# Optimization experiments

Hardware: AMD Instinct MI355X
Metric: run time of the kernel (lower is better)

Reference implementation:

```python
import jax, jax.numpy as jnp
import numpy as np

B, S, D_MODEL = 2, 2048, 1024
NUM_HEADS = 16
D_HEAD = D_MODEL // NUM_HEADS
THETA = 10000.0


def setup_inputs() -> dict:
    key = jax.random.key(0)
    ks = jax.random.split(key, 5)
    std = float(np.sqrt(2.0 / (D_MODEL + D_MODEL)))
    return {
        "x": jax.random.normal(ks[0], (B, S, D_MODEL), dtype=jnp.float32),
        "wq": jax.random.normal(ks[1], (D_MODEL, D_MODEL), dtype=jnp.float32) * std,
        "wk": jax.random.normal(ks[2], (D_MODEL, D_MODEL), dtype=jnp.float32) * std,
        "wv": jax.random.normal(ks[3], (D_MODEL, D_MODEL), dtype=jnp.float32) * std,
        "wo": jax.random.normal(ks[4], (D_MODEL, D_MODEL), dtype=jnp.float32) * std,
    }


def _apply_rope(x):
    # x: [b, h, s, d]; interleaved even/odd RoPE rotation
    d = x.shape[-1]
    s = x.shape[-2]
    inv_freq = 1.0 / (THETA ** (jnp.arange(0, d, 2, dtype=x.dtype) / d))  # [d/2]
    pos = jnp.arange(s, dtype=x.dtype)
    freqs = pos[:, None] * inv_freq[None, :]  # [s, d/2]
    cos, sin = jnp.cos(freqs), jnp.sin(freqs)
    x_even = x[..., 0::2]
    x_odd = x[..., 1::2]
    rot_even = x_even * cos - x_odd * sin
    rot_odd = x_even * sin + x_odd * cos
    # interleave back: stack pairs on a new trailing axis then flatten
    return jnp.stack([rot_even, rot_odd], axis=-1).reshape(x.shape)


def reference(x, wq, wk, wv, wo):
    b, s, _ = x.shape
    # Linear applies weight [d_out, d_in] as x @ W^T
    q = jnp.einsum('bsd,ed->bse', x, wq)
    k = jnp.einsum('bsd,ed->bse', x, wk)
    v = jnp.einsum('bsd,ed->bse', x, wv)
    # [b, s, h*dh] -> [b, h, s, dh]
    q = q.reshape(b, s, NUM_HEADS, D_HEAD).transpose(0, 2, 1, 3)
    k = k.reshape(b, s, NUM_HEADS, D_HEAD).transpose(0, 2, 1, 3)
    v = v.reshape(b, s, NUM_HEADS, D_HEAD).transpose(0, 2, 1, 3)
    q = _apply_rope(q)
    k = _apply_rope(k)
    scores = jnp.einsum('bhqd,bhkd->bhqk', q, k) / jnp.sqrt(jnp.asarray(D_HEAD, x.dtype))
    causal = jnp.tril(jnp.ones((s, s), dtype=bool))  # allowed positions
    scores = jnp.where(causal, scores, -jnp.inf)
    attn = jax.nn.softmax(scores, axis=-1)
    out = jnp.einsum('bhqk,bhkd->bhqd', attn, v)
    out = out.transpose(0, 2, 1, 3).reshape(b, s, NUM_HEADS * D_HEAD)
    return jnp.einsum('bsd,ed->bse', out, wo)
```

## Files before the change

kernel.cpp:

```cpp
#include <hip/hip_runtime.h>
#include <stdint.h>

typedef unsigned short u16;
typedef __attribute__((ext_vector_type(8))) short bf16x8;
typedef __attribute__((ext_vector_type(4))) short bf16x4;
typedef __attribute__((ext_vector_type(4))) float f32x4;
typedef __attribute__((ext_vector_type(4))) unsigned short u16x4;
typedef __attribute__((ext_vector_type(2))) unsigned u32x2;

#define S_ 2048
#define E_ 1024
#define QSCALE 0.18033688011112042f

__device__ __forceinline__ u16 f2bf(float f) {
  union { float f; unsigned u; } v; v.f = f;
  unsigned u = v.u;
  unsigned r = (u + 0x7FFFu + ((u >> 16) & 1u)) >> 16;
  return (u16)r;
}
__device__ __forceinline__ float bf2f(u16 h) {
  union { unsigned u; float f; } v; v.u = ((unsigned)h) << 16;
  return v.f;
}
__device__ __forceinline__ unsigned cvtpk(float a, float b) {
  unsigned r;
  asm("v_cvt_pk_bf16_f32 %0, %1, %2" : "=v"(r) : "v"(a), "v"(b));
  return r;
}
__device__ __forceinline__ bf16x4 pk4(float a, float b, float c, float d) {
  union { u32x2 u; bf16x4 v; } U;
  U.u[0] = cvtpk(a, b);
  U.u[1] = cvtpk(c, d);
  return U.v;
}

typedef __attribute__((address_space(3))) void lds_void;
__device__ __forceinline__ unsigned lds_off(void* p) {
  return (unsigned)(unsigned long long)(lds_void*)p;
}
__device__ __forceinline__ void glds16(const u16* g, u16* l) {
  __builtin_amdgcn_global_load_lds(
      (const __attribute__((address_space(1))) void*)g,
      (__attribute__((address_space(3))) void*)l, 16, 0, 0);
}

__global__ void k_cast5(const float* __restrict__ x,
                        const float* __restrict__ wq, const float* __restrict__ wk,
                        const float* __restrict__ wv, const float* __restrict__ wo,
                        u16* __restrict__ xb, u16* __restrict__ wqb, u16* __restrict__ wkb,
                        u16* __restrict__ wvb, u16* __restrict__ wob) {
  int i = blockIdx.x * blockDim.x + threadIdx.x;
  const float* src; u16* dst; int off;
  if (i < 1048576) { src = x; dst = xb; off = i; }
  else {
    int j = i - 1048576;
    int w = j >> 18; off = j & 262143;
    src = (w == 0) ? wq : (w == 1) ? wk : (w == 2) ? wv : wo;
    dst = (w == 0) ? wqb : (w == 1) ? wkb : (w == 2) ? wvb : wob;
  }
  float4 v = *((const float4*)src + off);
  u16x4 o;
  o.x = f2bf(v.x); o.y = f2bf(v.y); o.z = f2bf(v.z); o.w = f2bf(v.w);
  *((u16x4*)dst + off) = o;
}

__global__ __launch_bounds__(256) void k_gemm(
    const u16* __restrict__ A,
    const u16* __restrict__ W0, const u16* __restrict__ W1, const u16* __restrict__ W2,
    void* O0, void* O1, void* O2, int outF32)
{
  __shared__ __align__(16) u16 As[2][128 * 32];
  __shared__ __align__(16) u16 Ws[2][128 * 32];
  int tid = threadIdx.x;
  int wid = tid >> 6, lane = tid & 63;
  int lg = lane >> 4, lr = lane & 15;
  int wsel = blockIdx.y >> 3, nb = blockIdx.y & 7;
  const u16* W = (wsel == 0) ? W0 : ((wsel == 1) ? W1 : W2);
  void* O = (wsel == 0) ? O0 : ((wsel == 1) ? O1 : O2);
  int m0 = blockIdx.x * 128;
  int n0 = nb * 128;
  int wr = wid >> 1, wc = wid & 1;

  f32x4 acc[4][4];
#pragma unroll
  for (int m = 0; m < 4; m++)
#pragma unroll
    for (int n = 0; n < 4; n++) acc[m][n] = (f32x4){0.f, 0.f, 0.f, 0.f};

  int srow = tid >> 2;
  int schunk = (tid & 3) ^ ((tid >> 3) & 3);
  const u16* ag = A + (size_t)(m0 + srow) * 1024 + schunk * 8;
  const u16* wg = W + (size_t)(n0 + srow) * 1024 + schunk * 8;

  int buf = 0;
  glds16(ag, &As[0][tid * 8]);
  glds16(ag + 65536, &As[0][tid * 8 + 2048]);
  glds16(wg, &Ws[0][tid * 8]);
  glds16(wg + 65536, &Ws[0][tid * 8 + 2048]);
  __syncthreads();

  for (int kt = 0; kt < 1024; kt += 32) {
    if (kt + 32 < 1024) {
      glds16(ag + kt + 32, &As[buf ^ 1][tid * 8]);
      glds16(ag + kt + 32 + 65536, &As[buf ^ 1][tid * 8 + 2048]);
      glds16(wg + kt + 32, &Ws[buf ^ 1][tid * 8]);
      glds16(wg + kt + 32 + 65536, &Ws[buf ^ 1][tid * 8 + 2048]);
    }
    bf16x8 af[4], wf[4];
#pragma unroll
    for (int m = 0; m < 4; m++) {
      int row = wr * 64 + m * 16 + lr;
      af[m] = *(const bf16x8*)&As[buf][row * 32 + ((lg ^ ((row >> 1) & 3)) * 8)];
    }
#pragma unroll
    for (int n = 0; n < 4; n++) {
      int row = wc * 64 + n * 16 + lr;
      wf[n] = *(const bf16x8*)&Ws[buf][row * 32 + ((lg ^ ((row >> 1) & 3)) * 8)];
    }
    __builtin_amdgcn_s_setprio(1);
#pragma unroll
    for (int m = 0; m < 4; m++)
#pragma unroll
      for (int n = 0; n < 4; n++)
        acc[m][n] = __builtin_amdgcn_mfma_f32_16x16x32_bf16(af[m], wf[n], acc[m][n], 0, 0, 0);
    __builtin_amdgcn_s_setprio(0);
    __syncthreads();
    buf ^= 1;
  }

#pragma unroll
  for (int m = 0; m < 4; m++) {
    int gr = m0 + wr * 64 + m * 16 + lg * 4;
#pragma unroll
    for (int n = 0; n < 4; n++) {
      int gc = n0 + wc * 64 + n * 16 + lr;
#pragma unroll
      for (int r = 0; r < 4; r++) {
        if (outF32) ((float*)O)[(size_t)(gr + r) * 1024 + gc] = acc[m][n][r];
        else ((u16*)O)[(size_t)(gr + r) * 1024 + gc] = f2bf(acc[m][n][r]);
      }
    }
  }
}

__global__ void k_rope(u16* __restrict__ Q, u16* __restrict__ K) {
  int idx = blockIdx.x * blockDim.x + threadIdx.x;
  int p = idx & 511;
  int srow = idx >> 9;
  int s = srow & (S_ - 1);
  int i = p & 31;
  float ang = (float)s * exp2f(-0.415241012f * (float)i);
  float sn, c;
  __sincosf(ang, &sn, &c);
  unsigned* qp = (unsigned*)Q + idx;
  unsigned qv = *qp;
  float e = bf2f((u16)(qv & 0xffff)), o = bf2f((u16)(qv >> 16));
  float re = (e * c - o * sn) * QSCALE, ro = (e * sn + o * c) * QSCALE;
  *qp = cvtpk(re, ro);
  unsigned* kp = (unsigned*)K + idx;
  unsigned kv = *kp;
  e = bf2f((u16)(kv & 0xffff)); o = bf2f((u16)(kv >> 16));
  re = e * c - o * sn; ro = e * sn + o * c;
  *kp = cvtpk(re, ro);
}

__global__ __launch_bounds__(256) void k_attn(
    const u16* __restrict__ Q, const u16* __restrict__ K,
    const u16* __restrict__ V, u16* __restrict__ AO)
{
  __shared__ __align__(16) u16 Ks[64 * 64];
  __shared__ __align__(16) u16 Vs[64 * 64];
  int tid = threadIdx.x;
  int wid = tid >> 6, lane = tid & 63;
  int lg = lane >> 4, lr = lane & 15;
  int bh = blockIdx.x;
  int by = blockIdx.y;
  int b0 = by & 7, jj = by >> 3;
  int qb = (jj == 0) ? (b0 * 2)
         : (jj == 1) ? (31 - b0 * 2)
         : (jj == 2) ? (b0 * 2 + 1)
                     : (30 - b0 * 2);
  int q0 = qb * 64 + wid * 16;
  size_t base = (size_t)(bh >> 4) * (2048u * 1024u) + (size_t)(bh & 15) * 64;

  const u16* qrow = Q + base + (size_t)(q0 + lr) * 1024 + lg * 8;
  bf16x8 qf0 = *(const bf16x8*)(qrow);
  bf16x8 qf1 = *(const bf16x8*)(qrow + 32);

  int srow = tid >> 3;
  int sch = tid & 7;
  const u16* kg = K + base + (size_t)srow * 1024 + sch * 8;
  const u16* vg = V + base + (size_t)srow * 1024 + sch * 8;
  int kwb0 = ((srow)*128 + sch * 16) ^ ((srow & 7) << 4);
  int kwb1 = ((srow + 32) * 128 + sch * 16) ^ ((srow & 7) << 4);
  int vwi0 = (srow >> 4) * 1024 + (sch >> 1) * 256 + (srow & 15) * 16 + (sch & 1) * 8;
  int vwi1 = ((srow + 32) >> 4) * 1024 + (sch >> 1) * 256 + (srow & 15) * 16 + (sch & 1) * 8;

  bf16x8 kr0 = *(const bf16x8*)(kg);
  bf16x8 kr1 = *(const bf16x8*)(kg + 32 * 1024);
  bf16x8 vr0 = *(const bf16x8*)(vg);
  bf16x8 vr1 = *(const bf16x8*)(vg + 32 * 1024);
  const u16* kgp = kg + 64 * 1024;
  const u16* vgp = vg + 64 * 1024;

  float m = -1e30f, lsum = 0.f;
  f32x4 o[4];
#pragma unroll
  for (int cc = 0; cc < 4; cc++) o[cc] = (f32x4){0.f, 0.f, 0.f, 0.f};

  int qg = q0 + lr;
  int ntile = qb + 1;
  unsigned vrd = lds_off(Vs) + (unsigned)(lane * 8);

  for (int t = 0; t < ntile; ++t) {
    __syncthreads();
    *(bf16x8*)((char*)Ks + kwb0) = kr0;
    *(bf16x8*)((char*)Ks + kwb1) = kr1;
    *(bf16x8*)(&Vs[vwi0]) = vr0;
    *(bf16x8*)(&Vs[vwi1]) = vr1;
    __syncthreads();
    if (t + 1 < ntile) {
      kr0 = *(const bf16x8*)(kgp);
      kr1 = *(const bf16x8*)(kgp + 32 * 1024);
      vr0 = *(const bf16x8*)(vgp);
      vr1 = *(const bf16x8*)(vgp + 32 * 1024);
      kgp += 64 * 1024;
      vgp += 64 * 1024;
    }
    f32x4 sv[4];
    int kv0 = t * 64;
    __builtin_amdgcn_s_setprio(1);
#pragma unroll
    for (int sub = 0; sub < 4; ++sub) {
      int row = sub * 16 + lr;
      int swz = (row & 7) << 4;
      bf16x8 kf0 = *(const bf16x8*)((const char*)Ks + ((row * 128 + lg * 16) ^ swz));
      bf16x8 kf1 = *(const bf16x8*)((const char*)Ks + ((row * 128 + 64 + lg * 16) ^ swz));
      f32x4 z = (f32x4){0.f, 0.f, 0.f, 0.f};
      z = __builtin_amdgcn_mfma_f32_16x16x32_bf16(kf0, qf0, z, 0, 0, 0);
      sv[sub] = __builtin_amdgcn_mfma_f32_16x16x32_bf16(kf1, qf1, z, 0, 0, 0);
    }
    __builtin_amdgcn_s_setprio(0);
    if (t == ntile - 1) {
#pragma unroll
      for (int sub = 0; sub < 4; ++sub)
#pragma unroll
        for (int j = 0; j < 4; ++j) {
          int kvg = kv0 + sub * 16 + lg * 4 + j;
          sv[sub][j] = (kvg <= qg) ? sv[sub][j] : -1e30f;
        }
    }
    float tm = fmaxf(fmaxf(fmaxf(sv[0][0], sv[0][1]), fmaxf(sv[0][2], sv[0][3])),
                     fmaxf(fmaxf(sv[1][0], sv[1][1]), fmaxf(sv[1][2], sv[1][3])));
    tm = fmaxf(tm, fmaxf(fmaxf(fmaxf(sv[2][0], sv[2][1]), fmaxf(sv[2][2], sv[2][3])),
                         fmaxf(fmaxf(sv[3][0], sv[3][1]), fmaxf(sv[3][2], sv[3][3]))));
    tm = fmaxf(tm, __shfl_xor(tm, 16));
    tm = fmaxf(tm, __shfl_xor(tm, 32));
    if (!__all(tm <= m + 8.f)) {
      float mn = fmaxf(m, tm);
      float corr = __builtin_amdgcn_exp2f(m - mn);
      m = mn;
      lsum *= corr;
#pragma unroll
      for (int cc = 0; cc < 4; ++cc) {
        o[cc][0] *= corr; o[cc][1] *= corr; o[cc][2] *= corr; o[cc][3] *= corr;
      }
    }
    bf16x4 pb[4];
#pragma unroll
    for (int sub = 0; sub < 4; ++sub) {
      float p0 = __builtin_amdgcn_exp2f(sv[sub][0] - m);
      float p1 = __builtin_amdgcn_exp2f(sv[sub][1] - m);
      float p2 = __builtin_amdgcn_exp2f(sv[sub][2] - m);
      float p3 = __builtin_amdgcn_exp2f(sv[sub][3] - m);
      lsum += (p0 + p1) + (p2 + p3);
      pb[sub] = pk4(p0, p1, p2, p3);
    }
#pragma unroll
    for (int sub = 0; sub < 4; ++sub) {
      unsigned wa = vrd + (unsigned)(sub * 2048);
      bf16x4 va0, va1, va2, va3;
      asm volatile("ds_read_b64_tr_b16 %0, %1" : "=v"(va0) : "v"(wa));
      asm volatile("ds_read_b64_tr_b16 %0, %1 offset:512" : "=v"(va1) : "v"(wa));
      asm volatile("ds_read_b64_tr_b16 %0, %1 offset:1024" : "=v"(va2) : "v"(wa));
      asm volatile("ds_read_b64_tr_b16 %0, %1 offset:1536" : "=v"(va3) : "v"(wa));
      asm volatile("s_waitcnt lgkmcnt(0)" ::: "memory");
      __builtin_amdgcn_sched_barrier(0);
      __builtin_amdgcn_s_setprio(1);
      o[0] = __builtin_amdgcn_mfma_f32_16x16x16bf16_1k(va0, pb[sub], o[0], 0, 0, 0);
      o[1] = __builtin_amdgcn_mfma_f32_16x16x16bf16_1k(va1, pb[sub], o[1], 0, 0, 0);
      o[2] = __builtin_amdgcn_mfma_f32_16x16x16bf16_1k(va2, pb[sub], o[2], 0, 0, 0);
      o[3] = __builtin_amdgcn_mfma_f32_16x16x16bf16_1k(va3, pb[sub], o[3], 0, 0, 0);
      __builtin_amdgcn_s_setprio(0);
    }
  }

  float lt = lsum + __shfl_xor(lsum, 16);
  lt += __shfl_xor(lt, 32);
  float inv = 1.0f / lt;
  u16* orow = AO + base + (size_t)(q0 + lr) * 1024;
#pragma unroll
  for (int cc = 0; cc < 4; cc++) {
    u32x2 pk;
    pk[0] = cvtpk(o[cc][0] * inv, o[cc][1] * inv);
    pk[1] = cvtpk(o[cc][2] * inv, o[cc][3] * inv);
    *(u32x2*)&orow[cc * 16 + lg * 4] = pk;
  }
}

extern "C" void kernel_launch(void* const* d_in, const int* in_sizes, int n_in,
                              void* d_out, int out_size, void* d_ws, size_t ws_size,
                              hipStream_t stream) {
  const float* x = (const float*)d_in[0];
  const float* wq = (const float*)d_in[1];
  const float* wk = (const float*)d_in[2];
  const float* wv = (const float*)d_in[3];
  const float* wo = (const float*)d_in[4];

  char* ws = (char*)d_ws;
  u16* xb  = (u16*)(ws);
  u16* wqb = (u16*)(ws + 8388608);
  u16* wkb = (u16*)(ws + 10485760);
  u16* wvb = (u16*)(ws + 12582912);
  u16* wob = (u16*)(ws + 14680064);
  u16* Qb  = (u16*)(ws + 16777216);
  u16* Kb  = (u16*)(ws + 25165824);
  u16* Vb  = (u16*)(ws + 33554432);
  u16* AO  = (u16*)(ws + 41943040);

  k_cast5<<<8192, 256, 0, stream>>>(x, wq, wk, wv, wo, xb, wqb, wkb, wvb, wob);
  k_gemm<<<dim3(32, 24), 256, 0, stream>>>(xb, wqb, wkb, wvb, Qb, Kb, Vb, 0);
  k_rope<<<8192, 256, 0, stream>>>(Qb, Kb);
  k_attn<<<dim3(32, 32), 256, 0, stream>>>(Qb, Kb, Vb, AO);
  k_gemm<<<dim3(32, 8), 256, 0, stream>>>(AO, wob, wob, wob, d_out, d_out, d_out, 1);
}
```

Measured before the change: 119.1 us.

## Split causal attention KV range into two halves and merge partial softmax results

Each query block's causal KV tiles are now split into two halves handled by separate workgroups, doubling the attention grid. Each half writes an unnormalized bf16 output plus its running max and sum. A new merge kernel rescales and combines the two partials into the final attention output. The goal is more parallelism and a shorter tail from the longest causal rows. The cost is an extra launch, extra global traffic for the partials, and bf16 rounding of unnormalized accumulators. Freed workspace regions (the casted x and wq buffers) are reused to hold the partials.

```diff
diff --git a/kernel.cpp b/kernel.cpp
--- a/kernel.cpp
+++ b/kernel.cpp
@@ -7,6 +7,7 @@
 typedef __attribute__((ext_vector_type(4))) float f32x4;
 typedef __attribute__((ext_vector_type(4))) unsigned short u16x4;
 typedef __attribute__((ext_vector_type(2))) unsigned u32x2;
+typedef __attribute__((ext_vector_type(4))) unsigned u32x4;
 
 #define S_ 2048
 #define E_ 1024
@@ -166,7 +167,8 @@
 
 __global__ __launch_bounds__(256) void k_attn(
     const u16* __restrict__ Q, const u16* __restrict__ K,
-    const u16* __restrict__ V, u16* __restrict__ AO)
+    const u16* __restrict__ V, u16* __restrict__ AO,
+    u16* __restrict__ P0o, float* __restrict__ P0ml, float* __restrict__ P1ml)
 {
   __shared__ __align__(16) u16 Ks[64 * 64];
   __shared__ __align__(16) u16 Vs[64 * 64];
@@ -175,13 +177,31 @@
   int lg = lane >> 4, lr = lane & 15;
   int bh = blockIdx.x;
   int by = blockIdx.y;
-  int b0 = by & 7, jj = by >> 3;
-  int qb = (jj == 0) ? (b0 * 2)
-         : (jj == 1) ? (31 - b0 * 2)
-         : (jj == 2) ? (b0 * 2 + 1)
-                     : (30 - b0 * 2);
+  int qb = 31 - (by >> 1);
+  int part = by & 1;
+  int ntile = qb + 1;
+  int h = ntile >> 1;
+  int t0 = part ? h : 0;
+  int t1 = part ? ntile : h;
   int q0 = qb * 64 + wid * 16;
   size_t base = (size_t)(bh >> 4) * (2048u * 1024u) + (size_t)(bh & 15) * 64;
+  int mlbase = ((bh >> 4) * 2048) * 16 + (bh & 15);
+
+  u16* Oraw = part ? AO : P0o;
+  float* Pml = part ? P1ml : P0ml;
+
+  if (t0 == t1) {
+    int row = tid >> 2;
+    int col = (tid & 3) * 16;
+    u16* dst = P0o + base + (size_t)row * 1024 + col;
+#pragma unroll
+    for (int j = 0; j < 16; ++j) dst[j] = 0;
+    if (tid < 64) {
+      P0ml[(mlbase + tid * 16) * 2 + 0] = -1e30f;
+      P0ml[(mlbase + tid * 16) * 2 + 1] = 0.f;
+    }
+    return;
+  }
 
   const u16* qrow = Q + base + (size_t)(q0 + lr) * 1024 + lg * 8;
   bf16x8 qf0 = *(const bf16x8*)(qrow);
@@ -189,8 +209,8 @@
 
   int srow = tid >> 3;
   int sch = tid & 7;
-  const u16* kg = K + base + (size_t)srow * 1024 + sch * 8;
-  const u16* vg = V + base + (size_t)srow * 1024 + sch * 8;
+  const u16* kg = K + base + (size_t)srow * 1024 + sch * 8 + (size_t)t0 * 65536;
+  const u16* vg = V + base + (size_t)srow * 1024 + sch * 8 + (size_t)t0 * 65536;
   int kwb0 = ((srow)*128 + sch * 16) ^ ((srow & 7) << 4);
   int kwb1 = ((srow + 32) * 128 + sch * 16) ^ ((srow & 7) << 4);
   int vwi0 = (srow >> 4) * 1024 + (sch >> 1) * 256 + (srow & 15) * 16 + (sch & 1) * 8;
@@ -209,17 +229,16 @@
   for (int cc = 0; cc < 4; cc++) o[cc] = (f32x4){0.f, 0.f, 0.f, 0.f};
 
   int qg = q0 + lr;
-  int ntile = qb + 1;
   unsigned vrd = lds_off(Vs) + (unsigned)(lane * 8);
 
-  for (int t = 0; t < ntile; ++t) {
+  for (int t = t0; t < t1; ++t) {
     __syncthreads();
     *(bf16x8*)((char*)Ks + kwb0) = kr0;
     *(bf16x8*)((char*)Ks + kwb1) = kr1;
     *(bf16x8*)(&Vs[vwi0]) = vr0;
     *(bf16x8*)(&Vs[vwi1]) = vr1;
     __syncthreads();
-    if (t + 1 < ntile) {
+    if (t + 1 < t1) {
       kr0 = *(const bf16x8*)(kgp);
       kr1 = *(const bf16x8*)(kgp + 32 * 1024);
       vr0 = *(const bf16x8*)(vgp);
@@ -297,15 +316,44 @@
 
   float lt = lsum + __shfl_xor(lsum, 16);
   lt += __shfl_xor(lt, 32);
-  float inv = 1.0f / lt;
-  u16* orow = AO + base + (size_t)(q0 + lr) * 1024;
+  u16* orow = Oraw + base + (size_t)(q0 + lr) * 1024;
 #pragma unroll
   for (int cc = 0; cc < 4; cc++) {
     u32x2 pk;
-    pk[0] = cvtpk(o[cc][0] * inv, o[cc][1] * inv);
-    pk[1] = cvtpk(o[cc][2] * inv, o[cc][3] * inv);
+    pk[0] = cvtpk(o[cc][0], o[cc][1]);
+    pk[1] = cvtpk(o[cc][2], o[cc][3]);
     *(u32x2*)&orow[cc * 16 + lg * 4] = pk;
   }
+  if (lg == 0) {
+    int r2 = (mlbase + (q0 + lr) * 16) * 2;
+    Pml[r2] = m;
+    Pml[r2 + 1] = lt;
+  }
+}
+
+__global__ void k_merge(u16* __restrict__ AO, const u16* __restrict__ P0o,
+                        const float* __restrict__ P0ml, const float* __restrict__ P1ml) {
+  int idx = blockIdx.x * blockDim.x + threadIdx.x;
+  int r = idx >> 3;
+  int d0 = (idx & 7) * 8;
+  float m0 = P0ml[r * 2], l0 = P0ml[r * 2 + 1];
+  float m1 = P1ml[r * 2], l1 = P1ml[r * 2 + 1];
+  float M = fmaxf(m0, m1);
+  float a0 = __builtin_amdgcn_exp2f(m0 - M);
+  float a1 = __builtin_amdgcn_exp2f(m1 - M);
+  float inv = 1.0f / (l0 * a0 + l1 * a1);
+  float s0 = a0 * inv, s1 = a1 * inv;
+  size_t off = (size_t)(r >> 4) * 1024 + (size_t)(r & 15) * 64 + d0;
+  bf16x8 v0 = *(const bf16x8*)(P0o + off);
+  bf16x8 v1 = *(const bf16x8*)(AO + off);
+  u32x4 outw;
+#pragma unroll
+  for (int j = 0; j < 4; ++j) {
+    float f0 = bf2f((u16)v0[2 * j]) * s0 + bf2f((u16)v1[2 * j]) * s1;
+    float f1 = bf2f((u16)v0[2 * j + 1]) * s0 + bf2f((u16)v1[2 * j + 1]) * s1;
+    outw[j] = cvtpk(f0, f1);
+  }
+  *(u32x4*)(AO + off) = outw;
 }
 
 extern "C" void kernel_launch(void* const* d_in, const int* in_sizes, int n_in,
@@ -327,10 +375,14 @@
   u16* Kb  = (u16*)(ws + 25165824);
   u16* Vb  = (u16*)(ws + 33554432);
   u16* AO  = (u16*)(ws + 41943040);
+  u16*   P0o  = (u16*)(ws);
+  float* P0ml = (float*)(ws + 8388608);
+  float* P1ml = (float*)(ws + 9437184);
 
   k_cast5<<<8192, 256, 0, stream>>>(x, wq, wk, wv, wo, xb, wqb, wkb, wvb, wob);
   k_gemm<<<dim3(32, 24), 256, 0, stream>>>(xb, wqb, wkb, wvb, Qb, Kb, Vb, 0);
   k_rope<<<8192, 256, 0, stream>>>(Qb, Kb);
-  k_attn<<<dim3(32, 32), 256, 0, stream>>>(Qb, Kb, Vb, AO);
+  k_attn<<<dim3(32, 64), 256, 0, stream>>>(Qb, Kb, Vb, AO, P0o, P0ml, P1ml);
+  k_merge<<<2048, 256, 0, stream>>>(AO, P0o, P0ml, P1ml);
   k_gemm<<<dim3(32, 8), 256, 0, stream>>>(AO, wob, wob, wob, d_out, d_out, d_out, 1);
 }
```

After: 119.7 us. No clear change (+0.6%).
